# Kernel optimization log

Measured on AMD Instinct MI355X. Metric: run time of the kernel, lower is better.

The kernel has to match this reference:

```python
import jax, jax.numpy as jnp
import numpy as np

EPS = 1e-12  # torch F.normalize eps


def setup_inputs() -> dict:
    key = jax.random.key(0)
    ks = jax.random.split(key, 6)
    B, N, P, H = 32, 512, 8, 300
    node_attr = jax.random.normal(ks[0], (B, N, P, H), dtype=jnp.float32)
    edge_attr = jax.random.normal(ks[1], (B, 1, 1, H), dtype=jnp.float32)  # unused for ins_id=0
    instruction = jax.random.normal(ks[2], (B, H), dtype=jnp.float32)
    distribution = jax.random.uniform(ks[3], (B, N), dtype=jnp.float32)  # unused for ins_id=0
    node_prop_similarities = jax.random.uniform(ks[4], (B, P), dtype=jnp.float32)
    node_mask = jnp.zeros((B, N), dtype=jnp.float32)
    # weight_node_properties initialized as stacked identities; perturb to be nontrivial
    W_node = jnp.tile(jnp.eye(H, dtype=jnp.float32)[None], (P, 1, 1)) \
        + 0.02 * jax.random.normal(ks[5], (P, H, H), dtype=jnp.float32)
    w_state = jnp.ones((H,), dtype=jnp.float32)  # weight_state_score init = ones
    return {
        "node_attr": node_attr,
        "edge_attr": edge_attr,
        "instruction": instruction,
        "distribution": distribution,
        "ins_id": 0,
        "node_prop_similarities": node_prop_similarities,
        "node_mask": node_mask,
        "W_node": W_node,
        "w_state": w_state,
    }


def reference(node_attr, edge_attr, instruction, distribution, ins_id,
              node_prop_similarities, node_mask, W_node, w_state):
    # n_ins=3, ins_id=0 branch of NSMCell.forward
    # node_attr: (B,N,P,H) -> (B,P,N,H)
    x = jnp.transpose(node_attr, (0, 2, 1, 3))
    # broadcast-multiply instruction, then per-property matmul with W_node[p]
    y = instruction[:, None, None, :] * x                      # (B,P,N,H)
    z = jnp.einsum('bpnh,phk->bpnk', y, W_node)                # (B,P,N,H)
    z = z * node_prop_similarities[:, :, None, None]           # weight by property similarity
    # torch F.normalize default dim=1 -> L2-normalize over the P axis
    norm = jnp.sqrt(jnp.sum(z * z, axis=1, keepdims=True))
    z = z / jnp.maximum(norm, EPS)
    s = jnp.sum(z, axis=1)                                     # (B,N,H) sum over P
    node_scores = jax.nn.elu(s)                                # dropout p=0 -> identity
    scores = jnp.einsum('bnh,h->bn', node_scores, w_state)     # (B,N)
    return jax.nn.softmax(scores + node_mask, axis=1)
```

## Files before the change

### kernel.cpp

```cpp
#include <hip/hip_runtime.h>

#define B 32
#define N 512
#define P 8
#define H 300
#define HP 320
#define EPSN 1e-12f
#define NT 32
#define NB (N / NT)
#define SAP 328

typedef _Float16 f16x8 __attribute__((ext_vector_type(8)));
typedef float f32x4 __attribute__((ext_vector_type(4)));

__global__ __launch_bounds__(256)
void nsm_prep_w(const float* __restrict__ W, _Float16* __restrict__ wfrag)
{
    const int gid  = blockIdx.x * 256 + threadIdx.x;
    const int fb   = gid >> 6;
    const int lane = gid & 63;
    const int p  = fb / 200;
    const int rm = fb % 200;
    const int ht = rm / 20;
    const int kt = rm % 20;
    const int k  = kt * 16 + (lane & 15);
    const int h0 = ht * 32 + (lane >> 4) * 8;

    f16x8 v;
    #pragma unroll
    for (int j = 0; j < 8; ++j) {
        int h = h0 + j;
        float wv = (h < H && k < H) ? W[((size_t)p * H + h) * H + k] : 0.f;
        v[j] = (_Float16)wv;
    }
    *(f16x8*)(wfrag + (size_t)fb * 512 + (size_t)lane * 8) = v;
}

__global__ __launch_bounds__(256)
void nsm_prep_a(const float* __restrict__ node_attr,
                const float* __restrict__ instruction,
                _Float16* __restrict__ afrag)
{
    __shared__ _Float16 sA[NT * SAP];

    const int t  = threadIdx.x;
    const int nb = blockIdx.x;
    const int b  = blockIdx.y;
    const int p  = blockIdx.z;
    const int r  = t >> 3;
    const int cs = t & 7;

    const float* srcA = node_attr + ((size_t)((b * N + nb * NT + r) * P + p)) * H;
    const float* ins  = instruction + (size_t)b * H;

    #pragma unroll
    for (int i = 0; i < 10; ++i) {
        int s = cs + i * 8;
        int h = s * 4;
        _Float16 o0 = (_Float16)0.f, o1 = o0, o2 = o0, o3 = o0;
        if (s < 75) {
            float4 v  = *(const float4*)(srcA + h);
            float4 sc = *(const float4*)(ins + h);
            o0 = (_Float16)(v.x * sc.x);
            o1 = (_Float16)(v.y * sc.y);
            o2 = (_Float16)(v.z * sc.z);
            o3 = (_Float16)(v.w * sc.w);
        }
        sA[r * SAP + h]     = o0;
        sA[r * SAP + h + 1] = o1;
        sA[r * SAP + h + 2] = o2;
        sA[r * SAP + h + 3] = o3;
    }
    __syncthreads();

    const int w = t >> 6;
    const int l = t & 63;
    const size_t unit_base = ((size_t)(b * NB + nb) * P + p) * 20;
    #pragma unroll
    for (int uu = 0; uu < 5; ++uu) {
        int u  = w + uu * 4;
        int ht = u >> 1;
        int nt = u & 1;
        f16x8 v = *(const f16x8*)&sA[(nt * 16 + (l & 15)) * SAP + ht * 32 + (l >> 4) * 8];
        *(f16x8*)(afrag + (unit_base + u) * 512 + (size_t)l * 8) = v;
    }
}

__global__ __launch_bounds__(256, 2)
void nsm_scores_mfma(const _Float16* __restrict__ afrag,
                     const _Float16* __restrict__ wfrag,
                     const float* __restrict__ nps,
                     const float* __restrict__ w_state,
                     float* __restrict__ scores)
{
    const int t  = threadIdx.x;
    const int nb = blockIdx.x;
    const int b  = blockIdx.y;
    const int w  = t >> 6;
    const int l  = t & 63;

    const _Float16* Ab = afrag + ((size_t)(b * NB + nb) * P) * 10240 + (size_t)l * 8;
    const _Float16* Wb = wfrag + (size_t)(w * 5) * 512 + (size_t)l * 8;

    f32x4 S1[2][5], S2[2][5];
    #pragma unroll
    for (int nt = 0; nt < 2; ++nt)
        #pragma unroll
        for (int kt = 0; kt < 5; ++kt) {
            S1[nt][kt] = (f32x4){0.f, 0.f, 0.f, 0.f};
            S2[nt][kt] = (f32x4){0.f, 0.f, 0.f, 0.f};
        }

    for (int p = 0; p < P; ++p) {
        const _Float16* Ap = Ab + (size_t)p * 10240;
        const _Float16* Wp = Wb + (size_t)p * 102400;

        f32x4 acc[2][5];
        #pragma unroll
        for (int nt = 0; nt < 2; ++nt)
            #pragma unroll
            for (int kt = 0; kt < 5; ++kt)
                acc[nt][kt] = (f32x4){0.f, 0.f, 0.f, 0.f};

        #pragma unroll
        for (int ht = 0; ht < 10; ++ht) {
            f16x8 a0 = *(const f16x8*)(Ap + ht * 1024);
            f16x8 a1 = *(const f16x8*)(Ap + ht * 1024 + 512);
            #pragma unroll
            for (int kt = 0; kt < 5; ++kt) {
                f16x8 wf = *(const f16x8*)(Wp + ht * 10240 + kt * 512);
                acc[0][kt] = __builtin_amdgcn_mfma_f32_16x16x32_f16(a0, wf, acc[0][kt], 0, 0, 0);
                acc[1][kt] = __builtin_amdgcn_mfma_f32_16x16x32_f16(a1, wf, acc[1][kt], 0, 0, 0);
            }
        }

        const float sim = nps[b * P + p];
        #pragma unroll
        for (int nt = 0; nt < 2; ++nt)
            #pragma unroll
            for (int kt = 0; kt < 5; ++kt) {
                f32x4 z = acc[nt][kt] * sim;
                S1[nt][kt] += z;
                S2[nt][kt] += z * z;
            }
    }

    #pragma unroll
    for (int nt = 0; nt < 2; ++nt) {
        #pragma unroll
        for (int j = 0; j < 4; ++j) {
            float part = 0.f;
            #pragma unroll
            for (int kt = 0; kt < 5; ++kt) {
                int k = w * 80 + kt * 16 + (l & 15);
                if (k < H) {
                    float s1 = S1[nt][kt][j];
                    float s2 = S2[nt][kt][j];
                    float denom = fmaxf(sqrtf(s2), EPSN);
                    float v = s1 / denom;
                    float e = v > 0.f ? v : expm1f(v);
                    part += e * w_state[k];
                }
            }
            part += __shfl_xor(part, 1, 16);
            part += __shfl_xor(part, 2, 16);
            part += __shfl_xor(part, 4, 16);
            part += __shfl_xor(part, 8, 16);
            if ((l & 15) == 0)
                atomicAdd(&scores[b * N + nb * NT + nt * 16 + (l >> 4) * 4 + j], part);
        }
    }
}

__global__ __launch_bounds__(256)
void nsm_softmax_kernel(float* __restrict__ out, const float* __restrict__ mask)
{
    __shared__ float redm[4];
    __shared__ float reds[4];
    const int b = blockIdx.x;
    const int t = threadIdx.x;

    float v0 = out[b * N + t]       + mask[b * N + t];
    float v1 = out[b * N + 256 + t] + mask[b * N + 256 + t];

    float m = fmaxf(v0, v1);
    m = fmaxf(m, __shfl_xor(m, 1, 64));
    m = fmaxf(m, __shfl_xor(m, 2, 64));
    m = fmaxf(m, __shfl_xor(m, 4, 64));
    m = fmaxf(m, __shfl_xor(m, 8, 64));
    m = fmaxf(m, __shfl_xor(m, 16, 64));
    m = fmaxf(m, __shfl_xor(m, 32, 64));
    const int wave = t >> 6;
    const int lane = t & 63;
    if (lane == 0) redm[wave] = m;
    __syncthreads();
    m = fmaxf(fmaxf(redm[0], redm[1]), fmaxf(redm[2], redm[3]));

    float e0 = expf(v0 - m);
    float e1 = expf(v1 - m);
    float s = e0 + e1;
    s += __shfl_xor(s, 1, 64);
    s += __shfl_xor(s, 2, 64);
    s += __shfl_xor(s, 4, 64);
    s += __shfl_xor(s, 8, 64);
    s += __shfl_xor(s, 16, 64);
    s += __shfl_xor(s, 32, 64);
    if (lane == 0) reds[wave] = s;
    __syncthreads();
    s = reds[0] + reds[1] + reds[2] + reds[3];

    out[b * N + t]       = e0 / s;
    out[b * N + 256 + t] = e1 / s;
}

extern "C" void kernel_launch(void* const* d_in, const int* in_sizes, int n_in,
                              void* d_out, int out_size, void* d_ws, size_t ws_size,
                              hipStream_t stream)
{
    const float* node_attr   = (const float*)d_in[0];
    const float* instruction = (const float*)d_in[2];
    const float* nps         = (const float*)d_in[5];
    const float* node_mask   = (const float*)d_in[6];
    const float* W_node      = (const float*)d_in[7];
    const float* w_state     = (const float*)d_in[8];
    float* out = (float*)d_out;

    _Float16* afrag = (_Float16*)d_ws;
    _Float16* wfrag = afrag + (size_t)B * NB * P * 20 * 512;

    nsm_prep_w<<<dim3(400), 256, 0, stream>>>(W_node, wfrag);
    nsm_prep_a<<<dim3(NB, B, P), 256, 0, stream>>>(node_attr, instruction, afrag);

    (void)hipMemsetAsync(out, 0, (size_t)B * N * sizeof(float), stream);

    dim3 grid(NB, B);
    nsm_scores_mfma<<<grid, 256, 0, stream>>>(afrag, wfrag, nps, w_state, out);
    nsm_softmax_kernel<<<dim3(B), 256, 0, stream>>>(out, node_mask);
}
```

Measured before the change: 335.2 us.

## Merge prep kernels, prefetch MFMA fragments, replace atomics with per-wave partials

Folds the weight and activation prep into one launch, with an extra z-slice converting W. Activation staging now writes 8-wide vectors into shared memory with a wider pad. The MFMA kernel double-buffers A and W fragments in registers so global loads overlap compute. It writes per-wave partial scores instead of using atomics, which removes the memset; the softmax kernel sums the four partials. The register prefetch adds register pressure, which could hurt occupancy.

```diff
diff --git a/kernel.cpp b/kernel.cpp
--- a/kernel.cpp
+++ b/kernel.cpp
@@ -4,85 +4,88 @@
 #define N 512
 #define P 8
 #define H 300
-#define HP 320
 #define EPSN 1e-12f
 #define NT 32
 #define NB (N / NT)
-#define SAP 328
+#define SAP 344
 
 typedef _Float16 f16x8 __attribute__((ext_vector_type(8)));
 typedef float f32x4 __attribute__((ext_vector_type(4)));
 
 __global__ __launch_bounds__(256)
-void nsm_prep_w(const float* __restrict__ W, _Float16* __restrict__ wfrag)
-{
-    const int gid  = blockIdx.x * 256 + threadIdx.x;
-    const int fb   = gid >> 6;
-    const int lane = gid & 63;
-    const int p  = fb / 200;
-    const int rm = fb % 200;
-    const int ht = rm / 20;
-    const int kt = rm % 20;
-    const int k  = kt * 16 + (lane & 15);
-    const int h0 = ht * 32 + (lane >> 4) * 8;
-
-    f16x8 v;
-    #pragma unroll
-    for (int j = 0; j < 8; ++j) {
-        int h = h0 + j;
-        float wv = (h < H && k < H) ? W[((size_t)p * H + h) * H + k] : 0.f;
-        v[j] = (_Float16)wv;
-    }
-    *(f16x8*)(wfrag + (size_t)fb * 512 + (size_t)lane * 8) = v;
-}
-
-__global__ __launch_bounds__(256)
-void nsm_prep_a(const float* __restrict__ node_attr,
-                const float* __restrict__ instruction,
-                _Float16* __restrict__ afrag)
-{
+void nsm_prep(const float* __restrict__ node_attr,
+              const float* __restrict__ instruction,
+              const float* __restrict__ W,
+              _Float16* __restrict__ afrag,
+              _Float16* __restrict__ wfrag)
+{
+    const int t = threadIdx.x;
+    const int z = blockIdx.z;
+
+    if (z == P) {
+        const int idx = blockIdx.y * NB + blockIdx.x;
+        const int fb  = idx * 4 + (t >> 6);
+        if (fb >= 1600) return;
+        const int lane = t & 63;
+        const int p  = fb / 200;
+        const int rm = fb % 200;
+        const int ht = rm / 20;
+        const int kt = rm % 20;
+        const int k  = kt * 16 + (lane & 15);
+        const int h0 = ht * 32 + (lane >> 4) * 8;
+        f16x8 v;
+        #pragma unroll
+        for (int j = 0; j < 8; ++j) {
+            int h = h0 + j;
+            float wv = (h < H && k < H) ? W[((size_t)p * H + h) * H + k] : 0.f;
+            v[j] = (_Float16)wv;
+        }
+        *(f16x8*)(wfrag + (size_t)fb * 512 + (size_t)lane * 8) = v;
+        return;
+    }
+
     __shared__ _Float16 sA[NT * SAP];
-
-    const int t  = threadIdx.x;
-    const int nb = blockIdx.x;
-    const int b  = blockIdx.y;
-    const int p  = blockIdx.z;
+    const int nb = blockIdx.x, b = blockIdx.y, p = z;
     const int r  = t >> 3;
-    const int cs = t & 7;
+    const int oc = t & 7;
 
     const float* srcA = node_attr + ((size_t)((b * N + nb * NT + r) * P + p)) * H;
     const float* ins  = instruction + (size_t)b * H;
 
     #pragma unroll
-    for (int i = 0; i < 10; ++i) {
-        int s = cs + i * 8;
-        int h = s * 4;
-        _Float16 o0 = (_Float16)0.f, o1 = o0, o2 = o0, o3 = o0;
-        if (s < 75) {
-            float4 v  = *(const float4*)(srcA + h);
-            float4 sc = *(const float4*)(ins + h);
-            o0 = (_Float16)(v.x * sc.x);
-            o1 = (_Float16)(v.y * sc.y);
-            o2 = (_Float16)(v.z * sc.z);
-            o3 = (_Float16)(v.w * sc.w);
-        }
-        sA[r * SAP + h]     = o0;
-        sA[r * SAP + h + 1] = o1;
-        sA[r * SAP + h + 2] = o2;
-        sA[r * SAP + h + 3] = o3;
+    for (int i = 0; i < 5; ++i) {
+        int o  = oc + i * 8;
+        int h0 = o * 8;
+        f16x8 v8;
+        #pragma unroll
+        for (int j = 0; j < 8; ++j) v8[j] = (_Float16)0.f;
+        if (o < 37) {
+            float4 va = *(const float4*)(srcA + h0);
+            float4 vb = *(const float4*)(srcA + h0 + 4);
+            float4 sa = *(const float4*)(ins + h0);
+            float4 sb = *(const float4*)(ins + h0 + 4);
+            v8[0] = (_Float16)(va.x * sa.x); v8[1] = (_Float16)(va.y * sa.y);
+            v8[2] = (_Float16)(va.z * sa.z); v8[3] = (_Float16)(va.w * sa.w);
+            v8[4] = (_Float16)(vb.x * sb.x); v8[5] = (_Float16)(vb.y * sb.y);
+            v8[6] = (_Float16)(vb.z * sb.z); v8[7] = (_Float16)(vb.w * sb.w);
+        } else if (o == 37) {
+            float4 va = *(const float4*)(srcA + h0);
+            float4 sa = *(const float4*)(ins + h0);
+            v8[0] = (_Float16)(va.x * sa.x); v8[1] = (_Float16)(va.y * sa.y);
+            v8[2] = (_Float16)(va.z * sa.z); v8[3] = (_Float16)(va.w * sa.w);
+        }
+        *(f16x8*)&sA[r * SAP + h0] = v8;
     }
     __syncthreads();
 
-    const int w = t >> 6;
-    const int l = t & 63;
-    const size_t unit_base = ((size_t)(b * NB + nb) * P + p) * 20;
+    const int w = t >> 6, l = t & 63;
+    const size_t ub = ((size_t)(b * NB + nb) * P + p) * 20;
     #pragma unroll
     for (int uu = 0; uu < 5; ++uu) {
         int u  = w + uu * 4;
-        int ht = u >> 1;
-        int nt = u & 1;
+        int ht = u >> 1, nt = u & 1;
         f16x8 v = *(const f16x8*)&sA[(nt * 16 + (l & 15)) * SAP + ht * 32 + (l >> 4) * 8];
-        *(f16x8*)(afrag + (unit_base + u) * 512 + (size_t)l * 8) = v;
+        *(f16x8*)(afrag + (ub + u) * 512 + (size_t)l * 8) = v;
     }
 }
 
@@ -91,7 +94,7 @@
                      const _Float16* __restrict__ wfrag,
                      const float* __restrict__ nps,
                      const float* __restrict__ w_state,
-                     float* __restrict__ scores)
+                     float* __restrict__ pscore)
 {
     const int t  = threadIdx.x;
     const int nb = blockIdx.x;
@@ -111,10 +114,17 @@
             S2[nt][kt] = (f32x4){0.f, 0.f, 0.f, 0.f};
         }
 
+    f16x8 abuf[2][2], wbuf[2][5];
+    #pragma unroll
+    for (int s = 0; s < 2; ++s) {
+        abuf[s][0] = *(const f16x8*)(Ab + s * 1024);
+        abuf[s][1] = *(const f16x8*)(Ab + s * 1024 + 512);
+        #pragma unroll
+        for (int kt = 0; kt < 5; ++kt)
+            wbuf[s][kt] = *(const f16x8*)(Wb + (size_t)s * 10240 + kt * 512);
+    }
+
     for (int p = 0; p < P; ++p) {
-        const _Float16* Ap = Ab + (size_t)p * 10240;
-        const _Float16* Wp = Wb + (size_t)p * 102400;
-
         f32x4 acc[2][5];
         #pragma unroll
         for (int nt = 0; nt < 2; ++nt)
@@ -124,13 +134,21 @@
 
         #pragma unroll
         for (int ht = 0; ht < 10; ++ht) {
-            f16x8 a0 = *(const f16x8*)(Ap + ht * 1024);
-            f16x8 a1 = *(const f16x8*)(Ap + ht * 1024 + 512);
+            const int sl = ht & 1;
             #pragma unroll
             for (int kt = 0; kt < 5; ++kt) {
-                f16x8 wf = *(const f16x8*)(Wp + ht * 10240 + kt * 512);
-                acc[0][kt] = __builtin_amdgcn_mfma_f32_16x16x32_f16(a0, wf, acc[0][kt], 0, 0, 0);
-                acc[1][kt] = __builtin_amdgcn_mfma_f32_16x16x32_f16(a1, wf, acc[1][kt], 0, 0, 0);
+                acc[0][kt] = __builtin_amdgcn_mfma_f32_16x16x32_f16(abuf[sl][0], wbuf[sl][kt], acc[0][kt], 0, 0, 0);
+                acc[1][kt] = __builtin_amdgcn_mfma_f32_16x16x32_f16(abuf[sl][1], wbuf[sl][kt], acc[1][kt], 0, 0, 0);
+            }
+            if (ht < 8 || p < 7) {
+                const int s2 = p * 10 + ht + 2;
+                const _Float16* Ap2 = Ab + (size_t)s2 * 1024;
+                const _Float16* Wp2 = Wb + (size_t)s2 * 10240;
+                abuf[sl][0] = *(const f16x8*)(Ap2);
+                abuf[sl][1] = *(const f16x8*)(Ap2 + 512);
+                #pragma unroll
+                for (int kt = 0; kt < 5; ++kt)
+                    wbuf[sl][kt] = *(const f16x8*)(Wp2 + kt * 512);
             }
         }
 
@@ -166,22 +184,31 @@
             part += __shfl_xor(part, 2, 16);
             part += __shfl_xor(part, 4, 16);
             part += __shfl_xor(part, 8, 16);
-            if ((l & 15) == 0)
-                atomicAdd(&scores[b * N + nb * NT + nt * 16 + (l >> 4) * 4 + j], part);
+            if ((l & 15) == 0) {
+                int row = nt * 16 + (l >> 4) * 4 + j;
+                pscore[(size_t)w * (B * N) + (size_t)b * N + nb * NT + row] = part;
+            }
         }
     }
 }
 
 __global__ __launch_bounds__(256)
-void nsm_softmax_kernel(float* __restrict__ out, const float* __restrict__ mask)
+void nsm_softmax_kernel(const float* __restrict__ pscore,
+                        const float* __restrict__ mask,
+                        float* __restrict__ out)
 {
     __shared__ float redm[4];
     __shared__ float reds[4];
     const int b = blockIdx.x;
     const int t = threadIdx.x;
 
-    float v0 = out[b * N + t]       + mask[b * N + t];
-    float v1 = out[b * N + 256 + t] + mask[b * N + 256 + t];
+    float v0 = mask[b * N + t];
+    float v1 = mask[b * N + 256 + t];
+    #pragma unroll
+    for (int w = 0; w < 4; ++w) {
+        v0 += pscore[(size_t)w * (B * N) + b * N + t];
+        v1 += pscore[(size_t)w * (B * N) + b * N + 256 + t];
+    }
 
     float m = fmaxf(v0, v1);
     m = fmaxf(m, __shfl_xor(m, 1, 64));
@@ -227,13 +254,10 @@
 
     _Float16* afrag = (_Float16*)d_ws;
     _Float16* wfrag = afrag + (size_t)B * NB * P * 20 * 512;
-
-    nsm_prep_w<<<dim3(400), 256, 0, stream>>>(W_node, wfrag);
-    nsm_prep_a<<<dim3(NB, B, P), 256, 0, stream>>>(node_attr, instruction, afrag);
-
-    (void)hipMemsetAsync(out, 0, (size_t)B * N * sizeof(float), stream);
-
-    dim3 grid(NB, B);
-    nsm_scores_mfma<<<grid, 256, 0, stream>>>(afrag, wfrag, nps, w_state, out);
-    nsm_softmax_kernel<<<dim3(B), 256, 0, stream>>>(out, node_mask);
-}
+    float*    pscore = (float*)(wfrag + 1600 * 512);
+
+    nsm_prep<<<dim3(NB, B, P + 1), 256, 0, stream>>>(node_attr, instruction,
+                                                     W_node, afrag, wfrag);
+    nsm_scores_mfma<<<dim3(NB, B), 256, 0, stream>>>(afrag, wfrag, nps, w_state, pscore);
+    nsm_softmax_kernel<<<dim3(B), 256, 0, stream>>>(pscore, node_mask, out);
+}
```

New measurement: 340.1 us. Within noise of the previous version (+1.5%).
